# Kernel tuning notes

Measured on AMD Instinct MI355X. Metric: run time of the kernel, lower is better.

The kernel has to match this reference:

```python
import jax, jax.numpy as jnp
import numpy as np

R = 200000
PAD = 14            # residue_pad_length (atom14)
ACD, ATD, RCD, RID = 32, 8, 32, 32
N_ATOM_CODES, N_ATOM_TYPES, N_RES_CODES = 38, 6, 21
MAX_SEQ = 1024
OUT_0E, OUT_1E = 128, 32
IN0 = PAD * ACD + PAD * ATD + RCD + RID  # 624 scalar (0e) input channels


def setup_inputs() -> dict:
    key = jax.random.key(0)
    ks = jax.random.split(key, 12)
    counts_np = (4 + (np.arange(R) % 11)).astype(np.int32)  # atoms per residue in [4,14]
    n_atoms = int(counts_np.sum())  # 1,799,991
    residue_index_atomwise = jnp.asarray(np.repeat(np.arange(R, dtype=np.int32), counts_np))
    return {
        "relative_coords": jax.random.normal(ks[0], (n_atoms, 3), dtype=jnp.float32),
        "atom_code_index": jax.random.randint(ks[1], (n_atoms,), 1, N_ATOM_CODES, dtype=jnp.int32),
        "atom_type_index": jax.random.randint(ks[2], (n_atoms,), 1, N_ATOM_TYPES, dtype=jnp.int32),
        "residue_index_atomwise": residue_index_atomwise,
        "counts": jnp.asarray(counts_np),
        "residue_code_index": jax.random.randint(ks[3], (R,), 1, N_RES_CODES, dtype=jnp.int32),
        "residue_sequence_index": jax.random.randint(ks[4], (R,), 0, MAX_SEQ, dtype=jnp.int32),
        "base_coords": jax.random.normal(ks[5], (R, 3), dtype=jnp.float32),
        "atom_code_table": jax.random.normal(ks[6], (N_ATOM_CODES, ACD), dtype=jnp.float32),
        "atom_type_table": jax.random.normal(ks[7], (N_ATOM_TYPES, ATD), dtype=jnp.float32),
        "residue_code_table": jax.random.normal(ks[8], (N_RES_CODES, RCD), dtype=jnp.float32),
        "residue_index_table": jax.random.normal(ks[9], (MAX_SEQ, RID), dtype=jnp.float32),
        "W0": jax.random.normal(ks[10], (IN0, OUT_0E), dtype=jnp.float32),
        "W1": jax.random.normal(ks[11], (PAD, OUT_1E), dtype=jnp.float32),
    }


def _ragged_to_padded(residue_index_atomwise, counts, relative_coords,
                      atom_code_index, atom_type_index):
    # Single O(atoms) scatter replacing the per-residue python loop.
    n_atoms = relative_coords.shape[0]
    nres = counts.shape[0]
    starts = jnp.concatenate([jnp.zeros((1,), counts.dtype), jnp.cumsum(counts)[:-1]])
    pos = jnp.arange(n_atoms, dtype=counts.dtype) - starts[residue_index_atomwise]
    mask = jnp.arange(PAD, dtype=counts.dtype)[None, :] < counts[:, None]  # [R, PAD]
    coords_pad = jnp.zeros((nres, PAD, 3), relative_coords.dtype).at[
        residue_index_atomwise, pos].set(relative_coords)
    codes_pad = jnp.zeros((nres, PAD), jnp.int32).at[residue_index_atomwise, pos].set(atom_code_index)
    types_pad = jnp.zeros((nres, PAD), jnp.int32).at[residue_index_atomwise, pos].set(atom_type_index)
    return coords_pad, codes_pad, types_pad, mask


def reference(relative_coords, atom_code_index, atom_type_index,
              residue_index_atomwise, counts, residue_code_index,
              residue_sequence_index, base_coords,
              atom_code_table, atom_type_table, residue_code_table,
              residue_index_table, W0, W1):
    nres = counts.shape[0]
    coords_pad, codes_pad, types_pad, mask = _ragged_to_padded(
        residue_index_atomwise, counts, relative_coords, atom_code_index, atom_type_index)
    # embedding lookups, masked at padded slots (as in the torch module)
    ac = atom_code_table[codes_pad] * mask[..., None]   # [R, PAD, ACD]
    at = atom_type_table[types_pad] * mask[..., None]   # [R, PAD, ATD]
    rc = residue_code_table[residue_code_index]         # [R, RCD]
    ri = residue_index_table[residue_sequence_index]    # [R, RID]
    scalars = jnp.concatenate(
        [ac.reshape(nres, -1), at.reshape(nres, -1), rc, ri], axis=-1)  # [R, IN0]
    # e3nn o3.Linear: per-irrep-type mixing with 1/sqrt(fan_in) normalization.
    y0 = (scalars @ W0) * (1.0 / jnp.sqrt(jnp.float32(IN0)))            # 0e -> 0e
    y1 = jnp.einsum('rmc,mn->rnc', coords_pad, W1) * (1.0 / jnp.sqrt(jnp.float32(PAD)))  # 1e -> 1e
    features = jnp.concatenate([y0, y1.reshape(nres, -1)], axis=-1)     # [R, 128 + 96]
    return base_coords, features
```

## Files before the change

kernel.cpp:

```cpp
#include <hip/hip_runtime.h>
#include <hip/hip_bf16.h>

#define PAD        14
#define ACD        32
#define ATD        8
#define RCD        32
#define RID        32
#define N_CODES    38
#define N_TYPES    6
#define NCT        (N_CODES * N_TYPES)
#define N_RES      21
#define MAX_SEQ    1024
#define IN0        624
#define OUT0       128
#define OUT1       32
#define FEAT       224

#define NROWS_TCT  (PAD * NCT)
#define ZROW       NROWS_TCT
#define ROW_RC0    (ZROW + 1)
#define ROW_RI0    (ROW_RC0 + N_RES)
#define NROWS_ALL  (ROW_RI0 + MAX_SEQ)

__device__ __constant__ const float NORM0 = 0.04003203845f;
__device__ __constant__ const float NORM1 = 0.26726124191f;

typedef float f32x2 __attribute__((ext_vector_type(2)));

#define SZ_W1N     (PAD * OUT1)

#define T2_SZ_TCT     (PAD * NCT * OUT0)
#define T2_OFF_TCT    0
#define T2_OFF_TRC    (T2_OFF_TCT + T2_SZ_TCT)
#define T2_SZ_TRC     (N_RES * OUT0)
#define T2_OFF_TRI    (T2_OFF_TRC + T2_SZ_TRC)
#define T2_SZ_TRI     (MAX_SEQ * OUT0)
#define T2_OFF_W1N    (T2_OFF_TRI + T2_SZ_TRI)
#define T2_OFF_STARTS (T2_OFF_W1N + SZ_W1N)

__device__ __forceinline__ unsigned short f2bf(float v) {
    __hip_bfloat16 h = __float2bfloat16(v);
    unsigned short u;
    __builtin_memcpy(&u, &h, 2);
    return u;
}
__device__ __forceinline__ float bf_lo(unsigned int d) { return __uint_as_float(d << 16); }
__device__ __forceinline__ float bf_hi(unsigned int d) { return __uint_as_float(d & 0xffff0000u); }

__global__ void build_starts(const int* __restrict__ resIdx, int n_atoms,
                             int* __restrict__ starts,
                             const float* __restrict__ baseIn,
                             float* __restrict__ outBase, int nbase) {
    int i = blockIdx.x * blockDim.x + threadIdx.x;
    if (i < nbase) outBase[i] = baseIn[i];
    if (i >= n_atoms) return;
    int r = resIdx[i];
    if (i == 0 || resIdx[i - 1] != r) starts[r] = i;
}

__global__ void build_tall_meta(
    const float* __restrict__ act, const float* __restrict__ att,
    const float* __restrict__ rct, const float* __restrict__ rit,
    const float* __restrict__ W0, const float* __restrict__ W1,
    __hip_bfloat16* __restrict__ Tall, float* __restrict__ W1n,
    const int* __restrict__ starts, const int* __restrict__ counts,
    const int* __restrict__ codeIdx, const int* __restrict__ typeIdx,
    const float* __restrict__ coords,
    const int* __restrict__ rcIdx, const int* __restrict__ rsIdx,
    unsigned short* __restrict__ meta, int R) {
    int b = blockIdx.x;
    if (b <= NROWS_ALL) {
        int o = threadIdx.x;
        if (o >= OUT0) return;
        float acc = 0.f;
        if (b < NROWS_TCT) {
            int m = b / NCT, ct = b % NCT, c = ct / N_TYPES, t = ct % N_TYPES;
            const float* wc = W0 + (size_t)(m * ACD) * OUT0 + o;
            const float* wt = W0 + (size_t)(PAD * ACD + m * ATD) * OUT0 + o;
#pragma unroll
            for (int j = 0; j < ACD; ++j) acc += act[c * ACD + j] * wc[(size_t)j * OUT0];
#pragma unroll
            for (int j = 0; j < ATD; ++j) acc += att[t * ATD + j] * wt[(size_t)j * OUT0];
            Tall[(size_t)b * OUT0 + o] = __float2bfloat16(acc * NORM0);
        } else if (b == ZROW) {
            Tall[(size_t)b * OUT0 + o] = __float2bfloat16(0.f);
        } else if (b < ROW_RC0 + N_RES) {
            int c = b - ROW_RC0;
            const float* w = W0 + (size_t)(PAD * ACD + PAD * ATD) * OUT0 + o;
#pragma unroll
            for (int j = 0; j < RCD; ++j) acc += rct[c * RCD + j] * w[(size_t)j * OUT0];
            Tall[(size_t)b * OUT0 + o] = __float2bfloat16(acc * NORM0);
        } else if (b < NROWS_ALL) {
            int s = b - ROW_RI0;
            const float* w = W0 + (size_t)(PAD * ACD + PAD * ATD + RCD) * OUT0 + o;
#pragma unroll
            for (int j = 0; j < RID; ++j) acc += rit[s * RID + j] * w[(size_t)j * OUT0];
            Tall[(size_t)b * OUT0 + o] = __float2bfloat16(acc * NORM0);
        } else {
            for (int i = o; i < PAD * OUT1; i += OUT0) W1n[i] = W1[i] * NORM1;
        }
        return;
    }
    int gid = (b - (NROWS_ALL + 1)) * 256 + threadIdx.x;
    int r = gid >> 4, slot = gid & 15;
    if (r >= R) return;
    unsigned short* mp = meta + (size_t)r * 64;
    if (slot < PAD) {
        int cnt = counts[r];
        int row = ZROW;
        float cx = 0.f, cy = 0.f, cz = 0.f;
        if (slot < cnt) {
            int a = starts[r] + slot;
            row = slot * NCT + codeIdx[a] * N_TYPES + typeIdx[a];
            cx = coords[3 * (size_t)a + 0];
            cy = coords[3 * (size_t)a + 1];
            cz = coords[3 * (size_t)a + 2];
        }
        mp[slot]      = (unsigned short)row;
        mp[16 + slot] = f2bf(cx);
        mp[32 + slot] = f2bf(cy);
        mp[48 + slot] = f2bf(cz);
    } else if (slot == 14) {
        mp[14] = (unsigned short)(ROW_RC0 + rcIdx[r]);
    } else {
        mp[15] = (unsigned short)(ROW_RI0 + rsIdx[r]);
    }
}

__global__ __launch_bounds__(256) void main_fast2(
    const int* __restrict__ meta32,
    const unsigned int* __restrict__ Tall,
    const float* __restrict__ W1n,
    float* __restrict__ outFeat, int R) {
    int lane   = threadIdx.x & 63;
    int lane32 = lane & 31;
    int wid    = threadIdx.x >> 6;
    int pr = __builtin_amdgcn_readfirstlane(blockIdx.x * 4 + wid);
    int r0 = pr * 2;
    if (r0 >= R) return;
    bool has1 = (r0 + 1) < R;

    float w14[PAD];
#pragma unroll
    for (int m = 0; m < PAD; ++m) w14[m] = W1n[m * OUT1 + lane32];

    const int* mp = meta32 + (size_t)r0 * 32;
    int md[64];
#pragma unroll
    for (int j = 0; j < 32; ++j) md[j] = mp[j];
    if (has1) {
#pragma unroll
        for (int j = 32; j < 64; ++j) md[j] = mp[j];
    } else {
#pragma unroll
        for (int j = 32; j < 64; ++j) md[j] = 0;
    }

    unsigned int t0[16], t1[16];
#pragma unroll
    for (int k = 0; k < 8; ++k) {
        unsigned int dw = (unsigned int)md[k];
        t0[2 * k]     = Tall[(size_t)(dw & 0xffffu) * 64 + lane];
        t0[2 * k + 1] = Tall[(size_t)(dw >> 16) * 64 + lane];
    }
    if (has1) {
#pragma unroll
        for (int k = 0; k < 8; ++k) {
            unsigned int dw = (unsigned int)md[32 + k];
            t1[2 * k]     = Tall[(size_t)(dw & 0xffffu) * 64 + lane];
            t1[2 * k + 1] = Tall[(size_t)(dw >> 16) * 64 + lane];
        }
    }

    float vx0 = 0.f, vy0 = 0.f, vz0 = 0.f;
    float vx1 = 0.f, vy1 = 0.f, vz1 = 0.f;
#pragma unroll
    for (int m = 0; m < PAD; ++m) {
        int dw = m >> 1;
        unsigned int xd0 = (unsigned int)md[8 + dw];
        unsigned int yd0 = (unsigned int)md[16 + dw];
        unsigned int zd0 = (unsigned int)md[24 + dw];
        float cx0 = (m & 1) ? bf_hi(xd0) : bf_lo(xd0);
        float cy0 = (m & 1) ? bf_hi(yd0) : bf_lo(yd0);
        float cz0 = (m & 1) ? bf_hi(zd0) : bf_lo(zd0);
        vx0 = fmaf(cx0, w14[m], vx0);
        vy0 = fmaf(cy0, w14[m], vy0);
        vz0 = fmaf(cz0, w14[m], vz0);
        unsigned int xd1 = (unsigned int)md[40 + dw];
        unsigned int yd1 = (unsigned int)md[48 + dw];
        unsigned int zd1 = (unsigned int)md[56 + dw];
        float cx1 = (m & 1) ? bf_hi(xd1) : bf_lo(xd1);
        float cy1 = (m & 1) ? bf_hi(yd1) : bf_lo(yd1);
        float cz1 = (m & 1) ? bf_hi(zd1) : bf_lo(zd1);
        vx1 = fmaf(cx1, w14[m], vx1);
        vy1 = fmaf(cy1, w14[m], vy1);
        vz1 = fmaf(cz1, w14[m], vz1);
    }

    float acx0 = 0.f, acy0 = 0.f;
#pragma unroll
    for (int j = 0; j < 16; ++j) { acx0 += bf_lo(t0[j]); acy0 += bf_hi(t0[j]); }

    float* fo0 = outFeat + (size_t)r0 * FEAT;
    f32x2 a0; a0.x = acx0; a0.y = acy0;
    __builtin_nontemporal_store(a0, reinterpret_cast<f32x2*>(fo0) + lane);
    if (lane < 32) {
        float* p = fo0 + OUT0 + 3 * lane32;
        __builtin_nontemporal_store(vx0, p + 0);
        __builtin_nontemporal_store(vy0, p + 1);
        __builtin_nontemporal_store(vz0, p + 2);
    }

    if (has1) {
        float acx1 = 0.f, acy1 = 0.f;
#pragma unroll
        for (int j = 0; j < 16; ++j) { acx1 += bf_lo(t1[j]); acy1 += bf_hi(t1[j]); }
        float* fo1 = fo0 + FEAT;
        f32x2 a1; a1.x = acx1; a1.y = acy1;
        __builtin_nontemporal_store(a1, reinterpret_cast<f32x2*>(fo1) + lane);
        if (lane < 32) {
            float* p = fo1 + OUT0 + 3 * lane32;
            __builtin_nontemporal_store(vx1, p + 0);
            __builtin_nontemporal_store(vy1, p + 1);
            __builtin_nontemporal_store(vz1, p + 2);
        }
    }
}

__global__ void build_tables_t2(const float* __restrict__ act, const float* __restrict__ att,
                                const float* __restrict__ rct, const float* __restrict__ rit,
                                const float* __restrict__ W0, const float* __restrict__ W1,
                                float* __restrict__ Tct, float* __restrict__ Trc,
                                float* __restrict__ Tri, float* __restrict__ W1n) {
    int b = blockIdx.x;
    int o = threadIdx.x;
    float acc = 0.f;
    if (b < PAD * NCT) {
        int m = b / NCT, ct = b % NCT, c = ct / N_TYPES, t = ct % N_TYPES;
        const float* wc = W0 + (size_t)(m * ACD) * OUT0 + o;
        const float* wt = W0 + (size_t)(PAD * ACD + m * ATD) * OUT0 + o;
#pragma unroll
        for (int j = 0; j < ACD; ++j) acc += act[c * ACD + j] * wc[(size_t)j * OUT0];
#pragma unroll
        for (int j = 0; j < ATD; ++j) acc += att[t * ATD + j] * wt[(size_t)j * OUT0];
        Tct[(size_t)b * OUT0 + o] = acc * NORM0;
    } else if (b < PAD * NCT + N_RES) {
        int c = b - PAD * NCT;
        const float* w = W0 + (size_t)(PAD * ACD + PAD * ATD) * OUT0 + o;
#pragma unroll
        for (int j = 0; j < RCD; ++j) acc += rct[c * RCD + j] * w[(size_t)j * OUT0];
        Trc[(size_t)c * OUT0 + o] = acc * NORM0;
    } else if (b < PAD * NCT + N_RES + MAX_SEQ) {
        int s = b - (PAD * NCT + N_RES);
        const float* w = W0 + (size_t)(PAD * ACD + PAD * ATD + RCD) * OUT0 + o;
#pragma unroll
        for (int j = 0; j < RID; ++j) acc += rit[s * RID + j] * w[(size_t)j * OUT0];
        Tri[(size_t)s * OUT0 + o] = acc * NORM0;
    } else {
        for (int i = o; i < PAD * OUT1; i += OUT0) W1n[i] = W1[i] * NORM1;
    }
}

__global__ __launch_bounds__(256) void main_t2(
    const float*  __restrict__ coords, const int* __restrict__ codeIdx,
    const int*    __restrict__ typeIdx, const int* __restrict__ counts,
    const int*    __restrict__ rcIdx, const int* __restrict__ rsIdx,
    const float*  __restrict__ W1n,
    const float*  __restrict__ Tct, const float* __restrict__ Trc,
    const float*  __restrict__ Tri, const int* __restrict__ starts,
    float* __restrict__ outFeat, int R, int n_atoms) {
    int wid  = threadIdx.x >> 6;
    int lane = threadIdx.x & 63;
    int r = __builtin_amdgcn_readfirstlane(blockIdx.x * 4 + wid);
    if (r >= R) return;
    int start = starts[r];
    int cnt   = counts[r];
    int rc    = rcIdx[r];
    int rs    = rsIdx[r];
    int lane32 = lane & 31;
    int ci = 1, ti = 1;
    float crd = 0.f;
    if (lane < PAD) {
        int a = min(start + lane, n_atoms - 1);
        ci = codeIdx[a];
        ti = typeIdx[a];
    }
    if (lane < 3 * PAD) {
        int i3 = min(start * 3 + lane, 3 * n_atoms - 1);
        crd = coords[i3];
    }
    const f32x2* Tct2 = reinterpret_cast<const f32x2*>(Tct);
    const f32x2* Trc2 = reinterpret_cast<const f32x2*>(Trc);
    const f32x2* Tri2 = reinterpret_cast<const f32x2*>(Tri);
    f32x2 a0 = Trc2[(size_t)rc * 64 + lane];
    f32x2 a1 = Tri2[(size_t)rs * 64 + lane];
    int cmax = max(cnt - 1, 0);
    f32x2 t[PAD];
#pragma unroll
    for (int m = 0; m < PAD; ++m) {
        int mm = min(m, cmax);
        int cd = __builtin_amdgcn_readlane(ci, mm);
        int tp = __builtin_amdgcn_readlane(ti, mm);
        t[m] = Tct2[(size_t)(mm * NCT + cd * N_TYPES + tp) * 64 + lane];
    }
    float acx = a0.x + a1.x;
    float acy = a0.y + a1.y;
    float vx = 0.f, vy = 0.f, vz = 0.f;
#pragma unroll
    for (int m = 0; m < PAD; ++m) {
        int mm = min(m, cmax);
        float msk = (m < cnt) ? 1.f : 0.f;
        acx = fmaf(t[m].x, msk, acx);
        acy = fmaf(t[m].y, msk, acy);
        float cx = __uint_as_float(__builtin_amdgcn_readlane(__float_as_uint(crd), 3 * mm + 0));
        float cy = __uint_as_float(__builtin_amdgcn_readlane(__float_as_uint(crd), 3 * mm + 1));
        float cz = __uint_as_float(__builtin_amdgcn_readlane(__float_as_uint(crd), 3 * mm + 2));
        float w  = W1n[m * OUT1 + lane32] * msk;
        vx = fmaf(cx, w, vx);
        vy = fmaf(cy, w, vy);
        vz = fmaf(cz, w, vz);
    }
    float* fo = outFeat + (size_t)r * FEAT;
    f32x2 accv; accv.x = acx; accv.y = acy;
    __builtin_nontemporal_store(accv, reinterpret_cast<f32x2*>(fo) + lane);
    if (lane < 32) {
        float* p = fo + OUT0 + 3 * lane32;
        __builtin_nontemporal_store(vx, p + 0);
        __builtin_nontemporal_store(vy, p + 1);
        __builtin_nontemporal_store(vz, p + 2);
    }
}

__global__ __launch_bounds__(128) void fallback_kernel(
    const float* __restrict__ coords, const int* __restrict__ codeIdx,
    const int* __restrict__ typeIdx, const int* __restrict__ resIdx,
    const int* __restrict__ counts, const int* __restrict__ rcIdx,
    const int* __restrict__ rsIdx, const float* __restrict__ baseIn,
    const float* __restrict__ act, const float* __restrict__ att,
    const float* __restrict__ rct, const float* __restrict__ rit,
    const float* __restrict__ W0, const float* __restrict__ W1,
    float* __restrict__ outBase, float* __restrict__ outFeat, int R, int n_atoms) {
    int r = blockIdx.x, tid = threadIdx.x;
    __shared__ float s[IN0];
    __shared__ int sh_start;
    if (tid == 0) {
        int lo = 0, hi = n_atoms;
        while (lo < hi) { int mid = (lo + hi) >> 1; if (resIdx[mid] < r) lo = mid + 1; else hi = mid; }
        sh_start = lo;
    }
    __syncthreads();
    int start = sh_start, cnt = counts[r];
    for (int j = tid; j < IN0; j += 128) {
        float v = 0.f;
        if (j < PAD * ACD) {
            int m = j >> 5, jj = j & 31;
            if (m < cnt) v = act[codeIdx[start + m] * ACD + jj];
        } else if (j < PAD * ACD + PAD * ATD) {
            int t = j - PAD * ACD; int m = t >> 3, jj = t & 7;
            if (m < cnt) v = att[typeIdx[start + m] * ATD + jj];
        } else if (j < PAD * ACD + PAD * ATD + RCD) {
            v = rct[rcIdx[r] * RCD + (j - PAD * ACD - PAD * ATD)];
        } else {
            v = rit[rsIdx[r] * RID + (j - PAD * ACD - PAD * ATD - RCD)];
        }
        s[j] = v;
    }
    __syncthreads();
    float accv = 0.f;
    for (int j = 0; j < IN0; ++j) accv += s[j] * W0[(size_t)j * OUT0 + tid];
    float* fo = outFeat + (size_t)r * FEAT;
    fo[tid] = accv * NORM0;
    if (tid < 96) {
        int n = tid / 3, c = tid % 3;
        float v = 0.f;
        for (int m = 0; m < cnt; ++m) v += coords[(size_t)(start + m) * 3 + c] * W1[m * OUT1 + n];
        fo[OUT0 + tid] = v * NORM1;
    }
    if (tid < 3) outBase[(size_t)r * 3 + tid] = baseIn[(size_t)r * 3 + tid];
}

extern "C" void kernel_launch(void* const* d_in, const int* in_sizes, int n_in,
                              void* d_out, int out_size, void* d_ws, size_t ws_size,
                              hipStream_t stream) {
    const float* coords = (const float*)d_in[0];
    const int*   codeIdx = (const int*)d_in[1];
    const int*   typeIdx = (const int*)d_in[2];
    const int*   resIdx  = (const int*)d_in[3];
    const int*   counts  = (const int*)d_in[4];
    const int*   rcIdx   = (const int*)d_in[5];
    const int*   rsIdx   = (const int*)d_in[6];
    const float* baseIn  = (const float*)d_in[7];
    const float* act     = (const float*)d_in[8];
    const float* att     = (const float*)d_in[9];
    const float* rct     = (const float*)d_in[10];
    const float* rit     = (const float*)d_in[11];
    const float* W0      = (const float*)d_in[12];
    const float* W1      = (const float*)d_in[13];

    int n_atoms = in_sizes[1];
    int R       = in_sizes[4];

    float* out     = (float*)d_out;
    float* outBase = out;
    float* outFeat = out + (size_t)R * 3;

    size_t tallBytes = (size_t)NROWS_ALL * OUT0 * 2;
    size_t w1nOff    = tallBytes;
    size_t startsOff = w1nOff + (size_t)SZ_W1N * 4;
    size_t metaOff   = (startsOff + (size_t)R * 4 + 255) & ~(size_t)255;
    size_t needFast  = metaOff + ((size_t)R + 1) * 128;
    size_t needT2    = (size_t)(T2_OFF_STARTS + R) * 4;

    if (ws_size >= needFast) {
        char* wsb = (char*)d_ws;
        __hip_bfloat16* Tall   = (__hip_bfloat16*)wsb;
        unsigned int*   TallU  = (unsigned int*)wsb;
        float*          W1n    = (float*)(wsb + w1nOff);
        int*            starts = (int*)(wsb + startsOff);
        unsigned short* meta   = (unsigned short*)(wsb + metaOff);
        int*            meta32 = (int*)(wsb + metaOff);

        build_starts<<<(n_atoms + 255) / 256, 256, 0, stream>>>(
            resIdx, n_atoms, starts, baseIn, outBase, R * 3);
        int metaBlocks = (int)(((size_t)R * 16 + 255) / 256);
        build_tall_meta<<<(NROWS_ALL + 1) + metaBlocks, 256, 0, stream>>>(
            act, att, rct, rit, W0, W1, Tall, W1n,
            starts, counts, codeIdx, typeIdx, coords, rcIdx, rsIdx, meta, R);
        int pairs = (R + 1) / 2;
        main_fast2<<<(pairs + 3) / 4, 256, 0, stream>>>(
            meta32, TallU, W1n, outFeat, R);
    } else if (ws_size >= needT2) {
        float* ws     = (float*)d_ws;
        float* Tct    = ws + T2_OFF_TCT;
        float* Trc    = ws + T2_OFF_TRC;
        float* Tri    = ws + T2_OFF_TRI;
        float* W1n    = ws + T2_OFF_W1N;
        int*   starts = (int*)(ws + T2_OFF_STARTS);
        build_starts<<<(n_atoms + 255) / 256, 256, 0, stream>>>(
            resIdx, n_atoms, starts, baseIn, outBase, R * 3);
        int nrows = PAD * NCT + N_RES + MAX_SEQ + 1;
        build_tables_t2<<<nrows, OUT0, 0, stream>>>(act, att, rct, rit, W0, W1,
                                                    Tct, Trc, Tri, W1n);
        main_t2<<<(R + 3) / 4, 256, 0, stream>>>(
            coords, codeIdx, typeIdx, counts, rcIdx, rsIdx, W1n,
            Tct, Trc, Tri, starts, outFeat, R, n_atoms);
    } else {
        fallback_kernel<<<R, 128, 0, stream>>>(
            coords, codeIdx, typeIdx, resIdx, counts, rcIdx, rsIdx, baseIn,
            act, att, rct, rit, W0, W1, outBase, outFeat, R, n_atoms);
    }
}
```

Baseline: 80.84 us.

## Split y1 into its own kernel reading fp32 coords; shrink meta to row indices

Coordinate handling moves out of the meta build and the main kernel into a separate y1_kernel. That kernel loads each residue's contiguous fp32 coords with one wave and broadcasts them with readlane. The per-residue meta record shrinks from 128 to 32 bytes because it now holds only row indices, which cuts meta write and read traffic and drops the bf16 rounding of coords. In exchange there is an extra kernel launch, the y1 and y0 outputs are written by separate passes, and starts/counts are read again.

```diff
diff --git a/kernel.cpp b/kernel.cpp
--- a/kernel.cpp
+++ b/kernel.cpp
@@ -29,6 +29,8 @@
 
 #define SZ_W1N     (PAD * OUT1)
 
+#define META_DW    8
+
 #define T2_SZ_TCT     (PAD * NCT * OUT0)
 #define T2_OFF_TCT    0
 #define T2_OFF_TRC    (T2_OFF_TCT + T2_SZ_TCT)
@@ -38,12 +40,6 @@
 #define T2_OFF_W1N    (T2_OFF_TRI + T2_SZ_TRI)
 #define T2_OFF_STARTS (T2_OFF_W1N + SZ_W1N)
 
-__device__ __forceinline__ unsigned short f2bf(float v) {
-    __hip_bfloat16 h = __float2bfloat16(v);
-    unsigned short u;
-    __builtin_memcpy(&u, &h, 2);
-    return u;
-}
 __device__ __forceinline__ float bf_lo(unsigned int d) { return __uint_as_float(d << 16); }
 __device__ __forceinline__ float bf_hi(unsigned int d) { return __uint_as_float(d & 0xffff0000u); }
 
@@ -65,7 +61,6 @@
     __hip_bfloat16* __restrict__ Tall, float* __restrict__ W1n,
     const int* __restrict__ starts, const int* __restrict__ counts,
     const int* __restrict__ codeIdx, const int* __restrict__ typeIdx,
-    const float* __restrict__ coords,
     const int* __restrict__ rcIdx, const int* __restrict__ rsIdx,
     unsigned short* __restrict__ meta, int R) {
     int b = blockIdx.x;
@@ -104,22 +99,15 @@
     int gid = (b - (NROWS_ALL + 1)) * 256 + threadIdx.x;
     int r = gid >> 4, slot = gid & 15;
     if (r >= R) return;
-    unsigned short* mp = meta + (size_t)r * 64;
+    unsigned short* mp = meta + (size_t)r * 16;
     if (slot < PAD) {
         int cnt = counts[r];
         int row = ZROW;
-        float cx = 0.f, cy = 0.f, cz = 0.f;
         if (slot < cnt) {
             int a = starts[r] + slot;
             row = slot * NCT + codeIdx[a] * N_TYPES + typeIdx[a];
-            cx = coords[3 * (size_t)a + 0];
-            cy = coords[3 * (size_t)a + 1];
-            cz = coords[3 * (size_t)a + 2];
         }
-        mp[slot]      = (unsigned short)row;
-        mp[16 + slot] = f2bf(cx);
-        mp[32 + slot] = f2bf(cy);
-        mp[48 + slot] = f2bf(cz);
+        mp[slot] = (unsigned short)row;
     } else if (slot == 14) {
         mp[14] = (unsigned short)(ROW_RC0 + rcIdx[r]);
     } else {
@@ -127,33 +115,70 @@
     }
 }
 
-__global__ __launch_bounds__(256) void main_fast2(
+__global__ __launch_bounds__(256) void y1_kernel(
+    const float* __restrict__ coords, const int* __restrict__ starts,
+    const int* __restrict__ counts, const float* __restrict__ W1n,
+    float* __restrict__ outFeat, int R, int n_atoms) {
+    int wid  = threadIdx.x >> 6;
+    int lane = threadIdx.x & 63;
+    int r = __builtin_amdgcn_readfirstlane(blockIdx.x * 4 + wid);
+    if (r >= R) return;
+    int start = starts[r];
+    int cnt   = counts[r];
+    int lane32 = lane & 31;
+
+    float crd = 0.f;
+    if (lane < 3 * PAD) {
+        int i3 = min(start * 3 + lane, 3 * n_atoms - 1);
+        crd = coords[i3];
+    }
+    float w14[PAD];
+#pragma unroll
+    for (int m = 0; m < PAD; ++m) w14[m] = W1n[m * OUT1 + lane32];
+
+    int cmax = max(cnt - 1, 0);
+    float vx = 0.f, vy = 0.f, vz = 0.f;
+#pragma unroll
+    for (int m = 0; m < PAD; ++m) {
+        int mm = min(m, cmax);
+        float msk = (m < cnt) ? 1.f : 0.f;
+        float cx = __uint_as_float(__builtin_amdgcn_readlane(__float_as_uint(crd), 3 * mm + 0));
+        float cy = __uint_as_float(__builtin_amdgcn_readlane(__float_as_uint(crd), 3 * mm + 1));
+        float cz = __uint_as_float(__builtin_amdgcn_readlane(__float_as_uint(crd), 3 * mm + 2));
+        float w  = w14[m] * msk;
+        vx = fmaf(cx, w, vx);
+        vy = fmaf(cy, w, vy);
+        vz = fmaf(cz, w, vz);
+    }
+    if (lane < 32) {
+        float* p = outFeat + (size_t)r * FEAT + OUT0 + 3 * lane32;
+        __builtin_nontemporal_store(vx, p + 0);
+        __builtin_nontemporal_store(vy, p + 1);
+        __builtin_nontemporal_store(vz, p + 2);
+    }
+}
+
+__global__ __launch_bounds__(256) void main_y0(
     const int* __restrict__ meta32,
     const unsigned int* __restrict__ Tall,
-    const float* __restrict__ W1n,
     float* __restrict__ outFeat, int R) {
-    int lane   = threadIdx.x & 63;
-    int lane32 = lane & 31;
-    int wid    = threadIdx.x >> 6;
+    int lane = threadIdx.x & 63;
+    int wid  = threadIdx.x >> 6;
     int pr = __builtin_amdgcn_readfirstlane(blockIdx.x * 4 + wid);
     int r0 = pr * 2;
     if (r0 >= R) return;
     bool has1 = (r0 + 1) < R;
 
-    float w14[PAD];
-#pragma unroll
-    for (int m = 0; m < PAD; ++m) w14[m] = W1n[m * OUT1 + lane32];
-
-    const int* mp = meta32 + (size_t)r0 * 32;
-    int md[64];
-#pragma unroll
-    for (int j = 0; j < 32; ++j) md[j] = mp[j];
+    const int* mp = meta32 + (size_t)r0 * META_DW;
+    int md[16];
+#pragma unroll
+    for (int j = 0; j < 8; ++j) md[j] = mp[j];
     if (has1) {
 #pragma unroll
-        for (int j = 32; j < 64; ++j) md[j] = mp[j];
+        for (int j = 8; j < 16; ++j) md[j] = mp[j];
     } else {
 #pragma unroll
-        for (int j = 32; j < 64; ++j) md[j] = 0;
+        for (int j = 8; j < 16; ++j) md[j] = 0;
     }
 
     unsigned int t0[16], t1[16];
@@ -166,37 +191,12 @@
     if (has1) {
 #pragma unroll
         for (int k = 0; k < 8; ++k) {
-            unsigned int dw = (unsigned int)md[32 + k];
+            unsigned int dw = (unsigned int)md[8 + k];
             t1[2 * k]     = Tall[(size_t)(dw & 0xffffu) * 64 + lane];
             t1[2 * k + 1] = Tall[(size_t)(dw >> 16) * 64 + lane];
         }
     }
 
-    float vx0 = 0.f, vy0 = 0.f, vz0 = 0.f;
-    float vx1 = 0.f, vy1 = 0.f, vz1 = 0.f;
-#pragma unroll
-    for (int m = 0; m < PAD; ++m) {
-        int dw = m >> 1;
-        unsigned int xd0 = (unsigned int)md[8 + dw];
-        unsigned int yd0 = (unsigned int)md[16 + dw];
-        unsigned int zd0 = (unsigned int)md[24 + dw];
-        float cx0 = (m & 1) ? bf_hi(xd0) : bf_lo(xd0);
-        float cy0 = (m & 1) ? bf_hi(yd0) : bf_lo(yd0);
-        float cz0 = (m & 1) ? bf_hi(zd0) : bf_lo(zd0);
-        vx0 = fmaf(cx0, w14[m], vx0);
-        vy0 = fmaf(cy0, w14[m], vy0);
-        vz0 = fmaf(cz0, w14[m], vz0);
-        unsigned int xd1 = (unsigned int)md[40 + dw];
-        unsigned int yd1 = (unsigned int)md[48 + dw];
-        unsigned int zd1 = (unsigned int)md[56 + dw];
-        float cx1 = (m & 1) ? bf_hi(xd1) : bf_lo(xd1);
-        float cy1 = (m & 1) ? bf_hi(yd1) : bf_lo(yd1);
-        float cz1 = (m & 1) ? bf_hi(zd1) : bf_lo(zd1);
-        vx1 = fmaf(cx1, w14[m], vx1);
-        vy1 = fmaf(cy1, w14[m], vy1);
-        vz1 = fmaf(cz1, w14[m], vz1);
-    }
-
     float acx0 = 0.f, acy0 = 0.f;
 #pragma unroll
     for (int j = 0; j < 16; ++j) { acx0 += bf_lo(t0[j]); acy0 += bf_hi(t0[j]); }
@@ -204,12 +204,6 @@
     float* fo0 = outFeat + (size_t)r0 * FEAT;
     f32x2 a0; a0.x = acx0; a0.y = acy0;
     __builtin_nontemporal_store(a0, reinterpret_cast<f32x2*>(fo0) + lane);
-    if (lane < 32) {
-        float* p = fo0 + OUT0 + 3 * lane32;
-        __builtin_nontemporal_store(vx0, p + 0);
-        __builtin_nontemporal_store(vy0, p + 1);
-        __builtin_nontemporal_store(vz0, p + 2);
-    }
 
     if (has1) {
         float acx1 = 0.f, acy1 = 0.f;
@@ -218,12 +212,6 @@
         float* fo1 = fo0 + FEAT;
         f32x2 a1; a1.x = acx1; a1.y = acy1;
         __builtin_nontemporal_store(a1, reinterpret_cast<f32x2*>(fo1) + lane);
-        if (lane < 32) {
-            float* p = fo1 + OUT0 + 3 * lane32;
-            __builtin_nontemporal_store(vx1, p + 0);
-            __builtin_nontemporal_store(vy1, p + 1);
-            __builtin_nontemporal_store(vz1, p + 2);
-        }
     }
 }
 
@@ -408,7 +396,7 @@
     size_t w1nOff    = tallBytes;
     size_t startsOff = w1nOff + (size_t)SZ_W1N * 4;
     size_t metaOff   = (startsOff + (size_t)R * 4 + 255) & ~(size_t)255;
-    size_t needFast  = metaOff + ((size_t)R + 1) * 128;
+    size_t needFast  = metaOff + ((size_t)R + 1) * META_DW * 4;
     size_t needT2    = (size_t)(T2_OFF_STARTS + R) * 4;
 
     if (ws_size >= needFast) {
@@ -425,10 +413,12 @@
         int metaBlocks = (int)(((size_t)R * 16 + 255) / 256);
         build_tall_meta<<<(NROWS_ALL + 1) + metaBlocks, 256, 0, stream>>>(
             act, att, rct, rit, W0, W1, Tall, W1n,
-            starts, counts, codeIdx, typeIdx, coords, rcIdx, rsIdx, meta, R);
+            starts, counts, codeIdx, typeIdx, rcIdx, rsIdx, meta, R);
+        y1_kernel<<<(R + 3) / 4, 256, 0, stream>>>(
+            coords, starts, counts, W1n, outFeat, R, n_atoms);
         int pairs = (R + 1) / 2;
-        main_fast2<<<(pairs + 3) / 4, 256, 0, stream>>>(
-            meta32, TallU, W1n, outFeat, R);
+        main_y0<<<(pairs + 3) / 4, 256, 0, stream>>>(
+            meta32, TallU, outFeat, R);
     } else if (ws_size >= needT2) {
         float* ws     = (float*)d_ws;
         float* Tct    = ws + T2_OFF_TCT;
```

Measured after the change: 115.3 us. +42.7%, slower.
